# Performance work log

Measured on AMD Instinct MI355X. Metric: run time of the kernel, lower is better.

The kernel has to match this reference:

```python
import jax, jax.numpy as jnp
import numpy as np

D_MODEL = 512; D_INNER = 1024; D_STATE = 16; DT_RANK = 32; D_CONV = 4
N_LAYERS = 2; LSPP = 7; N_ROI = 2048; HIDDEN = 4096


def layer_norm(x, g, b, eps=1e-5):
    mu = x.mean(-1, keepdims=True)
    v = ((x - mu) ** 2).mean(-1, keepdims=True)
    return (x - mu) * jax.lax.rsqrt(v + eps) * g + b


def causal_dwconv(u, w, b):
    # u: [N,L,Di], w: [Di,K] depthwise, causal left-pad K-1
    x = jnp.transpose(u, (0, 2, 1))
    out = jax.lax.conv_general_dilated(x, w[:, None, :], (1,), [(D_CONV - 1, 0)],
                                       dimension_numbers=('NCH', 'OIH', 'NCH'),
                                       feature_group_count=D_INNER)
    return jnp.transpose(out, (0, 2, 1)) + b


def selective_scan(u, dt, A, B, C):
    # u, dt: [N,L,Di]; B, C: [N,L,S]; A: [Di,S]
    def step(h, xs):
        dt_t, B_t, C_t, u_t = xs
        dA = jnp.exp(dt_t[..., None] * A)                      # [N,Di,S]
        h = dA * h + (dt_t * u_t)[..., None] * B_t[:, None, :]
        return h, jnp.einsum('nds,ns->nd', h, C_t)
    h0 = jnp.zeros((u.shape[0], D_INNER, D_STATE), u.dtype)
    xs = (jnp.moveaxis(dt, 1, 0), jnp.moveaxis(B, 1, 0),
          jnp.moveaxis(C, 1, 0), jnp.moveaxis(u, 1, 0))
    _, ys = jax.lax.scan(step, h0, xs)
    return jnp.moveaxis(ys, 0, 1)                              # [N,L,Di]


def mamba_block(h, inw, cw, cb, xpw, dtw, dtb, Alog, Dp, ow):
    # decomposed bidirectional mamba ('dbm'): shared in_proj/gate, fwd+bwd scans summed
    xz = h @ inw.T                                             # [N,L,2*Di]
    xi, z = jnp.split(xz, 2, axis=-1)
    ys = []
    for d in range(2):
        u = xi if d == 0 else jnp.flip(xi, axis=1)
        u = jax.nn.silu(causal_dwconv(u, cw[d], cb[d]))
        dbl = u @ xpw[d].T                                     # [N,L,DT_RANK+2S]
        dtr = dbl[..., :DT_RANK]
        B = dbl[..., DT_RANK:DT_RANK + D_STATE]
        C = dbl[..., DT_RANK + D_STATE:]
        dt = jax.nn.softplus(dtr @ dtw[d].T + dtb[d])
        A = -jnp.exp(Alog[d])
        yd = selective_scan(u, dt, A, B, C) + u * Dp[d]
        ys.append(yd if d == 0 else jnp.flip(yd, axis=1))
    return ((ys[0] + ys[1]) * jax.nn.silu(z)) @ ow.T


def setup_inputs() -> dict:
    key = jax.random.key(0)
    ks = iter(jax.random.split(key, 40))
    rn = lambda shape, scale: jax.random.normal(next(ks), shape, dtype=jnp.float32) * scale
    inp = {}
    inp['x_flat'] = rn((N_ROI, D_MODEL * LSPP), 1.0)
    inp['conv_a_w'] = rn((256, 512, 3), (512 * 3) ** -0.5)
    inp['conv_p_w'] = rn((256, 512, 1), 512 ** -0.5)
    inp['se_w1'] = rn((32, 512), 512 ** -0.5)
    inp['se_b1'] = jnp.zeros((32,), jnp.float32)
    inp['se_w2'] = rn((512, 32), 32 ** -0.5)
    inp['se_b2'] = jnp.zeros((512,), jnp.float32)
    inp['ln_g'] = jnp.ones((N_LAYERS, D_MODEL), jnp.float32)
    inp['ln_b'] = jnp.zeros((N_LAYERS, D_MODEL), jnp.float32)
    inp['in_proj_w'] = rn((N_LAYERS, 2 * D_INNER, D_MODEL), D_MODEL ** -0.5)
    inp['conv_w'] = rn((N_LAYERS, 2, D_INNER, D_CONV), D_CONV ** -0.5)
    inp['conv_b'] = jnp.zeros((N_LAYERS, 2, D_INNER), jnp.float32)
    inp['x_proj_w'] = rn((N_LAYERS, 2, DT_RANK + 2 * D_STATE, D_INNER), D_INNER ** -0.5)
    inp['dt_proj_w'] = rn((N_LAYERS, 2, D_INNER, DT_RANK), DT_RANK ** -0.5)
    inp['dt_proj_b'] = rn((N_LAYERS, 2, D_INNER), 0.1) - 4.0
    inp['A_log'] = jnp.log(jnp.arange(1., D_STATE + 1., dtype=jnp.float32)) * jnp.ones((N_LAYERS, 2, D_INNER, D_STATE), jnp.float32)
    inp['D_param'] = jnp.ones((N_LAYERS, 2, D_INNER), jnp.float32)
    inp['out_proj_w'] = rn((N_LAYERS, D_MODEL, D_INNER), D_INNER ** -0.5)
    inp['out_ln_g'] = jnp.ones((D_MODEL,), jnp.float32)
    inp['out_ln_b'] = jnp.zeros((D_MODEL,), jnp.float32)
    inp['mlp_w1'] = rn((HIDDEN, D_MODEL), D_MODEL ** -0.5)
    inp['mlp_b1'] = jnp.zeros((HIDDEN,), jnp.float32)
    inp['mlp_w2'] = rn((HIDDEN, HIDDEN), HIDDEN ** -0.5)
    inp['mlp_b2'] = jnp.zeros((HIDDEN,), jnp.float32)
    return inp


def reference(x_flat, conv_a_w, conv_p_w, se_w1, se_b1, se_w2, se_b2, ln_g, ln_b,
              in_proj_w, conv_w, conv_b, x_proj_w, dt_proj_w, dt_proj_b, A_log,
              D_param, out_proj_w, out_ln_g, out_ln_b, mlp_w1, mlp_b1, mlp_w2, mlp_b2):
    N = x_flat.shape[0]
    x = x_flat.reshape(N, D_MODEL, LSPP)                       # [N,512,7]
    dn = ('NCH', 'OIH', 'NCH')
    # TSSE: strided conv branch + maxpool branch, concat, SE gating; L: 7 -> 4
    a = jax.nn.relu(jax.lax.conv_general_dilated(x, conv_a_w, (2,), [(1, 1)], dimension_numbers=dn))
    p = jax.lax.reduce_window(x, -jnp.inf, jax.lax.max, (1, 1, 3), (1, 1, 2), ((0, 0), (0, 0), (1, 1)))
    p = jax.nn.relu(jax.lax.conv_general_dilated(p, conv_p_w, (1,), [(0, 0)], dimension_numbers=dn))
    y = jnp.concatenate([a, p], axis=1)                        # [N,512,4]
    s = jax.nn.sigmoid(jax.nn.relu(y.mean(-1) @ se_w1.T + se_b1) @ se_w2.T + se_b2)
    y = y * s[:, :, None]
    # Mamba backbone: 2 pre-norm residual DBM blocks (mask is all-ones -> no-op)
    h = jnp.transpose(y, (0, 2, 1))                            # [N,L,512]
    for l in range(N_LAYERS):
        h = h + mamba_block(layer_norm(h, ln_g[l], ln_b[l]), in_proj_w[l], conv_w[l],
                            conv_b[l], x_proj_w[l], dt_proj_w[l], dt_proj_b[l],
                            A_log[l], D_param[l], out_proj_w[l])
    h = layer_norm(h, out_ln_g, out_ln_b)
    feat = h.mean(1)                                           # mean pool over time
    z1 = jax.nn.relu(feat @ mlp_w1.T + mlp_b1)
    return jax.nn.relu(z1 @ mlp_w2.T + mlp_b2)                 # [N,4096]
```

## Files before the change

### kernel.cpp

```cpp
#include <hip/hip_runtime.h>
#include <hip/hip_bf16.h>

typedef __hip_bfloat16 bf16;
typedef __attribute__((ext_vector_type(8))) short s16x8;
typedef __attribute__((ext_vector_type(4))) float f32x4;

__device__ __forceinline__ float u2f(unsigned short u){
  union { unsigned int i; float f; } v; v.i = ((unsigned int)u) << 16; return v.f;
}
__device__ __forceinline__ float bfu(bf16 x){ return __bfloat162float(x); }
__device__ __forceinline__ bf16  f2b(float x){ return __float2bfloat16(x); }

__device__ __forceinline__ void gload16(const void* g, void* l){
  __builtin_amdgcn_global_load_lds(
      (const __attribute__((address_space(1))) void*)g,
      (__attribute__((address_space(3))) void*)l, 16, 0, 0);
}

__device__ __forceinline__ float block_sum256(float v, float* red){
  #pragma unroll
  for (int o = 32; o > 0; o >>= 1) v += __shfl_down(v, o, 64);
  int lane = threadIdx.x & 63, wid = threadIdx.x >> 6;
  if (lane == 0) red[wid] = v;
  __syncthreads();
  float r = red[0] + red[1] + red[2] + red[3];
  __syncthreads();
  return r;
}

__global__ __launch_bounds__(256) void f2b4_kernel(
    const float4* __restrict__ in, ushort4* __restrict__ out, int n4)
{
  int stride = gridDim.x * 256;
  for (int i = blockIdx.x*256 + threadIdx.x; i < n4; i += stride){
    float4 v = in[i];
    ushort4 o;
    o.x = __bfloat16_as_ushort(f2b(v.x));
    o.y = __bfloat16_as_ushort(f2b(v.y));
    o.z = __bfloat16_as_ushort(f2b(v.z));
    o.w = __bfloat16_as_ushort(f2b(v.w));
    out[i] = o;
  }
}

__global__ __launch_bounds__(256) void xpw_pad_kernel(
    const float* __restrict__ xpw, bf16* __restrict__ out)
{
  int idx = blockIdx.x*256 + threadIdx.x;
  if (idx >= 524288) return;
  int l = idx >> 18, rem = idx & 262143, row = rem >> 10, c = rem & 1023;
  int d = row >> 7, r = row & 127;
  float v = (r < 64) ? xpw[(((size_t)l*2 + d)*64 + r)*1024 + c] : 0.f;
  out[idx] = f2b(v);
}

__global__ __launch_bounds__(256) void wdt_pad_kernel(
    const float* __restrict__ dtw, bf16* __restrict__ out)
{
  int idx = blockIdx.x*256 + threadIdx.x;
  if (idx >= 262144) return;
  int ld = idx >> 16, rem = idx & 65535, r = rem >> 6, c = rem & 63;
  float v = (c < 32) ? dtw[((size_t)ld*1024 + r)*32 + c] : 0.f;
  out[idx] = f2b(v);
}

__global__ __launch_bounds__(256) void atab_kernel(
    const float* __restrict__ Alog, float* __restrict__ Atab)
{
  int i = blockIdx.x*256 + threadIdx.x;
  if (i < 65536) Atab[i] = -__expf(Alog[i]) * 1.44269504088896f;
}

template<int ACT, int OMODE, bool HASBIAS>
__global__ __launch_bounds__(256) void mgemm_kernel(
    const bf16* __restrict__ A, const bf16* __restrict__ W,
    const float* __restrict__ bias, void* __restrict__ outp,
    int K, int ldo)
{
  __shared__ char lsA[16384];
  __shared__ char lsB[16384];
  const int tid = threadIdx.x;
  const int w = tid >> 6, l = tid & 63;
  const int nwg = gridDim.x * gridDim.y;
  const int lin = blockIdx.y * gridDim.x + blockIdx.x;
  const int cpx = nwg >> 3;
  const int swz = (lin & 7) * cpx + (lin >> 3);
  const int m0 = (swz % gridDim.x) * 128, n0 = (swz / gridDim.x) * 128;
  const int wr = w >> 1, wc = w & 1;
  const size_t ldb = (size_t)K * 2;
  const char* Ab = (const char*)A + (size_t)m0 * ldb;
  const char* Wb = (const char*)W + (size_t)n0 * ldb;

  const int srow = l >> 3;
  const int scb  = ((l & 7) ^ srow) << 4;
  const int fr = l & 15;
  const int fg = l >> 4;
  const int fsw = (fr & 7) << 4;

  f32x4 acc[4][4];
  #pragma unroll
  for (int m = 0; m < 4; ++m)
    #pragma unroll
    for (int n = 0; n < 4; ++n) acc[m][n] = (f32x4){0.f,0.f,0.f,0.f};

  const int nk = K >> 6;
  for (int kt = 0; kt < nk; ++kt){
    const char* As = Ab + (size_t)kt * 128;
    const char* Ws = Wb + (size_t)kt * 128;
    #pragma unroll
    for (int i = 0; i < 4; ++i){
      int row = (i*4 + w)*8 + srow;
      gload16(As + (size_t)row*ldb + scb, &lsA[(i*4 + w)*1024]);
    }
    #pragma unroll
    for (int i = 0; i < 4; ++i){
      int row = (i*4 + w)*8 + srow;
      gload16(Ws + (size_t)row*ldb + scb, &lsB[(i*4 + w)*1024]);
    }
    __syncthreads();

    s16x8 af[4][2], bfr[4][2];
    #pragma unroll
    for (int m = 0; m < 4; ++m){
      int row = wr*64 + m*16 + fr;
      af[m][0] = *(const s16x8*)&lsA[row*128 + (( 0 + fg*16) ^ fsw)];
      af[m][1] = *(const s16x8*)&lsA[row*128 + ((64 + fg*16) ^ fsw)];
    }
    #pragma unroll
    for (int n = 0; n < 4; ++n){
      int row = wc*64 + n*16 + fr;
      bfr[n][0] = *(const s16x8*)&lsB[row*128 + (( 0 + fg*16) ^ fsw)];
      bfr[n][1] = *(const s16x8*)&lsB[row*128 + ((64 + fg*16) ^ fsw)];
    }
    #pragma unroll
    for (int m = 0; m < 4; ++m)
      #pragma unroll
      for (int n = 0; n < 4; ++n){
        acc[m][n] = __builtin_amdgcn_mfma_f32_16x16x32_bf16(af[m][0], bfr[n][0], acc[m][n], 0, 0, 0);
        acc[m][n] = __builtin_amdgcn_mfma_f32_16x16x32_bf16(af[m][1], bfr[n][1], acc[m][n], 0, 0, 0);
      }
    __syncthreads();
  }

  const int orow0 = m0 + wr*64, ocol0 = n0 + wc*64;
  #pragma unroll
  for (int n = 0; n < 4; ++n){
    int col = ocol0 + n*16 + fr;
    float bv = HASBIAS ? bias[col] : 0.f;
    #pragma unroll
    for (int m = 0; m < 4; ++m){
      int rbase = orow0 + m*16 + fg*4;
      #pragma unroll
      for (int r = 0; r < 4; ++r){
        float v = acc[m][n][r] + bv;
        if (ACT == 1) v = fmaxf(v, 0.f);
        if (ACT == 2) v = (v > 20.f) ? v : log1pf(__expf(v));
        size_t oi = (size_t)(rbase + r) * ldo + col;
        if (OMODE == 0)      ((bf16*)outp)[oi] = f2b(v);
        else if (OMODE == 1) ((float*)outp)[oi] = v;
        else                 ((float*)outp)[oi] += v;
      }
    }
  }
}

__global__ __launch_bounds__(256) void bgemm_kernel(
    const bf16* __restrict__ A, const bf16* __restrict__ W,
    bf16* __restrict__ dtr_buf, float* __restrict__ dbl)
{
  __shared__ char lsA[16384];
  __shared__ char lsB[16384];
  const int tid = threadIdx.x;
  const int w = tid >> 6, l = tid & 63;
  const int nwg = gridDim.x * 2;
  const int lin = blockIdx.y * gridDim.x + blockIdx.x;
  const int cpx = nwg >> 3;
  const int swz = (lin & 7) * cpx + (lin >> 3);
  const int m0 = (swz % gridDim.x) * 128;
  const int d  = swz / gridDim.x;
  const int K = 1024;
  const int wr = w >> 1, wc = w & 1;
  const size_t ldb = (size_t)K * 2;
  const char* Ab = (const char*)(A + (size_t)d*8388608) + (size_t)m0 * ldb;
  const char* Wb = (const char*)(W + (size_t)d*131072);

  const int srow = l >> 3;
  const int scb  = ((l & 7) ^ srow) << 4;
  const int fr = l & 15;
  const int fg = l >> 4;
  const int fsw = (fr & 7) << 4;

  f32x4 acc[4][4];
  #pragma unroll
  for (int m = 0; m < 4; ++m)
    #pragma unroll
    for (int n = 0; n < 4; ++n) acc[m][n] = (f32x4){0.f,0.f,0.f,0.f};

  const int nk = K >> 6;
  for (int kt = 0; kt < nk; ++kt){
    const char* As = Ab + (size_t)kt * 128;
    const char* Ws = Wb + (size_t)kt * 128;
    #pragma unroll
    for (int i = 0; i < 4; ++i){
      int row = (i*4 + w)*8 + srow;
      gload16(As + (size_t)row*ldb + scb, &lsA[(i*4 + w)*1024]);
    }
    #pragma unroll
    for (int i = 0; i < 4; ++i){
      int row = (i*4 + w)*8 + srow;
      gload16(Ws + (size_t)row*ldb + scb, &lsB[(i*4 + w)*1024]);
    }
    __syncthreads();

    s16x8 af[4][2], bfr[4][2];
    #pragma unroll
    for (int m = 0; m < 4; ++m){
      int row = wr*64 + m*16 + fr;
      af[m][0] = *(const s16x8*)&lsA[row*128 + (( 0 + fg*16) ^ fsw)];
      af[m][1] = *(const s16x8*)&lsA[row*128 + ((64 + fg*16) ^ fsw)];
    }
    #pragma unroll
    for (int n = 0; n < 4; ++n){
      int row = wc*64 + n*16 + fr;
      bfr[n][0] = *(const s16x8*)&lsB[row*128 + (( 0 + fg*16) ^ fsw)];
      bfr[n][1] = *(const s16x8*)&lsB[row*128 + ((64 + fg*16) ^ fsw)];
    }
    #pragma unroll
    for (int m = 0; m < 4; ++m)
      #pragma unroll
      for (int n = 0; n < 4; ++n){
        acc[m][n] = __builtin_amdgcn_mfma_f32_16x16x32_bf16(af[m][0], bfr[n][0], acc[m][n], 0, 0, 0);
        acc[m][n] = __builtin_amdgcn_mfma_f32_16x16x32_bf16(af[m][1], bfr[n][1], acc[m][n], 0, 0, 0);
      }
    __syncthreads();
  }

  const int orow0 = m0 + wr*64, c0 = wc*64;
  #pragma unroll
  for (int n = 0; n < 4; ++n){
    int col = c0 + n*16 + fr;
    #pragma unroll
    for (int m = 0; m < 4; ++m){
      int rbase = orow0 + m*16 + fg*4;
      #pragma unroll
      for (int r = 0; r < 4; ++r){
        float v = acc[m][n][r];
        int row = rbase + r;
        if (col < 32)
          dtr_buf[((size_t)d*8192 + row)*64 + col] = f2b(v);
        else if (col < 64)
          dbl[(size_t)row*128 + d*64 + (col - 32)] = v;
        else if (col < 96)
          dtr_buf[((size_t)d*8192 + row)*64 + (col - 32)] = f2b(v);
      }
    }
  }
}

__global__ __launch_bounds__(256) void im2col_kernel(
    const float* __restrict__ x_flat, bf16* __restrict__ Aa, bf16* __restrict__ P)
{
  __shared__ float xs[512][8];
  const int n = blockIdx.x, tid = threadIdx.x;
  const float* xr = x_flat + (size_t)n * 3584;
  for (int i = tid; i < 3584; i += 256) xs[i / 7][i % 7] = xr[i];
  __syncthreads();
  bf16* Ar = Aa + (size_t)n * 4 * 1536;
  for (int i = tid; i < 6144; i += 256){
    int t = i / 1536, col = i - t*1536;
    int c = col / 3, kk = col - c*3;
    int p = 2*t - 1 + kk;
    float v = (p >= 0 && p < 7) ? xs[c][p] : 0.f;
    Ar[i] = f2b(v);
  }
  bf16* Pr = P + (size_t)n * 4 * 512;
  for (int i = tid; i < 2048; i += 256){
    int t = i >> 9, c = i & 511;
    int st = 2*t - 1;
    float m = -1e30f;
    #pragma unroll
    for (int k = 0; k < 3; ++k){ int p = st + k; if (p >= 0 && p < 7) m = fmaxf(m, xs[c][p]); }
    Pr[i] = f2b(m);
  }
}

__global__ __launch_bounds__(256) void se_kernel(
    const float* __restrict__ sw1, const float* __restrict__ sb1,
    const float* __restrict__ sw2, const float* __restrict__ sb2,
    float* __restrict__ h)
{
  __shared__ float yms[512];
  __shared__ float s1s[32];
  const int n = blockIdx.x, tid = threadIdx.x;
  float* hb = h + (size_t)n * 2048;
  for (int c = tid; c < 512; c += 256)
    yms[c] = 0.25f * (hb[c] + hb[512+c] + hb[1024+c] + hb[1536+c]);
  __syncthreads();
  {
    int o = tid >> 3, sl = tid & 7;
    const float* wr = sw1 + (size_t)o * 512 + sl*64;
    const float* ym = yms + sl*64;
    float a = 0.f;
    #pragma unroll 16
    for (int i = 0; i < 64; ++i) a += wr[i] * ym[i];
    a += __shfl_down(a, 4, 8);
    a += __shfl_down(a, 2, 8);
    a += __shfl_down(a, 1, 8);
    if (sl == 0) s1s[o] = fmaxf(a + sb1[o], 0.f);
  }
  __syncthreads();
  for (int c = tid; c < 512; c += 256){
    float a = sb2[c];
    const float* wr = sw2 + (size_t)c * 32;
    #pragma unroll
    for (int j = 0; j < 32; ++j) a += wr[j] * s1s[j];
    float s = 1.f / (1.f + __expf(-a));
    #pragma unroll
    for (int t = 0; t < 4; ++t) hb[t*512 + c] *= s;
  }
}

__global__ __launch_bounds__(256) void ln_kernel(
    const float* __restrict__ x, const float* __restrict__ g,
    const float* __restrict__ b, bf16* __restrict__ out)
{
  __shared__ float red[4];
  const int row = blockIdx.x, t = threadIdx.x;
  const float* xr = x + (size_t)row * 512;
  float v0 = xr[t], v1 = xr[t + 256];
  float s = block_sum256(v0 + v1, red);
  float mu = s * (1.f/512.f);
  float d0 = v0 - mu, d1 = v1 - mu;
  float sq = block_sum256(d0*d0 + d1*d1, red);
  float rstd = rsqrtf(sq * (1.f/512.f) + 1e-5f);
  out[(size_t)row*512 + t]       = f2b(d0*rstd*g[t]     + b[t]);
  out[(size_t)row*512 + t + 256] = f2b(d1*rstd*g[t+256] + b[t+256]);
}

__global__ __launch_bounds__(256) void finalln_kernel(
    const float* __restrict__ h, const float* __restrict__ g,
    const float* __restrict__ b, bf16* __restrict__ feat)
{
  __shared__ float red[4];
  const int n = blockIdx.x, t = threadIdx.x;
  float a0 = 0.f, a1 = 0.f;
  for (int tt = 0; tt < 4; ++tt){
    const float* xr = h + ((size_t)n*4 + tt)*512;
    float v0 = xr[t], v1 = xr[t+256];
    float s = block_sum256(v0 + v1, red);
    float mu = s * (1.f/512.f);
    float d0 = v0 - mu, d1 = v1 - mu;
    float sq = block_sum256(d0*d0 + d1*d1, red);
    float rstd = rsqrtf(sq * (1.f/512.f) + 1e-5f);
    a0 += d0*rstd*g[t]     + b[t];
    a1 += d1*rstd*g[t+256] + b[t+256];
  }
  feat[(size_t)n*512 + t]       = f2b(a0 * 0.25f);
  feat[(size_t)n*512 + t + 256] = f2b(a1 * 0.25f);
}

__global__ __launch_bounds__(256) void dwconv2_kernel(
    const bf16* __restrict__ xz, const float* __restrict__ cw,
    const float* __restrict__ cb, bf16* __restrict__ u)
{
  const int n = blockIdx.x;
  const int c4 = threadIdx.x * 4;
  ushort4 in4[4];
  #pragma unroll
  for (int t = 0; t < 4; ++t)
    in4[t] = *reinterpret_cast<const ushort4*>(&xz[((size_t)n*4 + t)*2048 + c4]);
  #pragma unroll
  for (int d = 0; d < 2; ++d){
    const float* cwd = cw + d*4096;
    const float* cbd = cb + d*1024;
    ushort4 out[4];
    #pragma unroll
    for (int j = 0; j < 4; ++j){
      float xa[4];
      #pragma unroll
      for (int t = 0; t < 4; ++t){
        int ts = d ? 3 - t : t;
        unsigned short us = j==0?in4[ts].x : j==1?in4[ts].y : j==2?in4[ts].z : in4[ts].w;
        xa[t] = u2f(us);
      }
      float4 wv = *reinterpret_cast<const float4*>(&cwd[(c4 + j)*4]);
      float bb = cbd[c4 + j];
      float o[4];
      o[0] = xa[0]*wv.w + bb;
      o[1] = xa[0]*wv.z + xa[1]*wv.w + bb;
      o[2] = xa[0]*wv.y + xa[1]*wv.z + xa[2]*wv.w + bb;
      o[3] = xa[0]*wv.x + xa[1]*wv.y + xa[2]*wv.z + xa[3]*wv.w + bb;
      #pragma unroll
      for (int t = 0; t < 4; ++t){
        float v = o[t];
        float sv = v / (1.f + __expf(-v));
        unsigned short us = __bfloat16_as_ushort(f2b(sv));
        if (j==0) out[t].x = us; else if (j==1) out[t].y = us;
        else if (j==2) out[t].z = us; else out[t].w = us;
      }
    }
    #pragma unroll
    for (int t = 0; t < 4; ++t)
      *reinterpret_cast<ushort4*>(&u[(size_t)d*8388608 + ((size_t)n*4 + t)*1024 + c4]) = out[t];
  }
}

__global__ __launch_bounds__(256) void scan2_kernel(
    const float* __restrict__ dbl, const bf16* __restrict__ dt2,
    const bf16* __restrict__ u, const bf16* __restrict__ xz,
    const float* __restrict__ Atab2, const float* __restrict__ Dp,
    bf16* __restrict__ gated)
{
  __shared__ float Bs[2][4][16], Cs[2][4][16];
  const int n = blockIdx.x, g = blockIdx.y, tid = threadIdx.x;
  {
    int t = tid >> 6, j = tid & 63;
    int d = j >> 5, jj = j & 31;
    float v = dbl[((size_t)n*4 + t)*128 + d*64 + jj];
    if (jj < 16) Bs[d][t][jj] = v; else Cs[d][t][jj-16] = v;
  }
  __syncthreads();
  const int c = g*256 + tid;
  const size_t base = (size_t)n*4*1024 + c;
  float yo0[4], yo1[4];
  float hs[16];
  {
    float A[16];
    const float4* ap = reinterpret_cast<const float4*>(Atab2 + (size_t)c*16);
    #pragma unroll
    for (int q = 0; q < 4; ++q){
      float4 v = ap[q];
      A[q*4+0]=v.x; A[q*4+1]=v.y; A[q*4+2]=v.z; A[q*4+3]=v.w;
    }
    const float Dpc = Dp[c];
    #pragma unroll
    for (int s = 0; s < 16; ++s) hs[s] = 0.f;
    #pragma unroll
    for (int t = 0; t < 4; ++t){
      float dtv = bfu(dt2[base + (size_t)t*1024]);
      float uv  = bfu(u  [base + (size_t)t*1024]);
      float du = dtv * uv;
      float yv = 0.f;
      #pragma unroll
      for (int s = 0; s < 16; ++s){
        float dA = __builtin_amdgcn_exp2f(dtv * A[s]);
        hs[s] = dA * hs[s] + du * Bs[0][t][s];
        yv += hs[s] * Cs[0][t][s];
      }
      yo0[t] = yv + uv * Dpc;
    }
  }
  {
    float A[16];
    const float4* ap = reinterpret_cast<const float4*>(Atab2 + 16384 + (size_t)c*16);
    #pragma unroll
    for (int q = 0; q < 4; ++q){
      float4 v = ap[q];
      A[q*4+0]=v.x; A[q*4+1]=v.y; A[q*4+2]=v.z; A[q*4+3]=v.w;
    }
    const float Dpc = Dp[1024 + c];
    #pragma unroll
    for (int s = 0; s < 16; ++s) hs[s] = 0.f;
    #pragma unroll
    for (int t = 0; t < 4; ++t){
      float dtv = bfu(dt2[8388608 + base + (size_t)t*1024]);
      float uv  = bfu(u  [8388608 + base + (size_t)t*1024]);
      float du = dtv * uv;
      float yv = 0.f;
      #pragma unroll
      for (int s = 0; s < 16; ++s){
        float dA = __builtin_amdgcn_exp2f(dtv * A[s]);
        hs[s] = dA * hs[s] + du * Bs[1][t][s];
        yv += hs[s] * Cs[1][t][s];
      }
      yo1[3 - t] = yv + uv * Dpc;
    }
  }
  #pragma unroll
  for (int t = 0; t < 4; ++t){
    float z = bfu(xz[(size_t)(n*4 + t)*2048 + 1024 + c]);
    float sv = z / (1.f + __expf(-z));
    gated[base + (size_t)t*1024] = f2b((yo0[t] + yo1[t]) * sv);
  }
}

extern "C" void kernel_launch(void* const* d_in, const int* in_sizes, int n_in,
                              void* d_out, int out_size, void* d_ws, size_t ws_size,
                              hipStream_t stream)
{
  const float* x_flat    = (const float*)d_in[0];
  const float* conv_a_w  = (const float*)d_in[1];
  const float* conv_p_w  = (const float*)d_in[2];
  const float* se_w1     = (const float*)d_in[3];
  const float* se_b1     = (const float*)d_in[4];
  const float* se_w2     = (const float*)d_in[5];
  const float* se_b2     = (const float*)d_in[6];
  const float* ln_g      = (const float*)d_in[7];
  const float* ln_b      = (const float*)d_in[8];
  const float* in_proj_w = (const float*)d_in[9];
  const float* conv_w    = (const float*)d_in[10];
  const float* conv_b    = (const float*)d_in[11];
  const float* x_proj_w  = (const float*)d_in[12];
  const float* dt_proj_w = (const float*)d_in[13];
  const float* dt_proj_b = (const float*)d_in[14];
  const float* A_log     = (const float*)d_in[15];
  const float* D_param   = (const float*)d_in[16];
  const float* out_proj_w= (const float*)d_in[17];
  const float* out_ln_g  = (const float*)d_in[18];
  const float* out_ln_b  = (const float*)d_in[19];
  const float* mlp_w1    = (const float*)d_in[20];
  const float* mlp_b1    = (const float*)d_in[21];
  const float* mlp_w2    = (const float*)d_in[22];
  const float* mlp_b2    = (const float*)d_in[23];

  char* ws = (char*)d_ws;
  const size_t OFF_H    = 0;
  const size_t OFF_HN   = OFF_H    + 16777216;
  const size_t OFF_XZ   = OFF_HN   + 8388608;
  const size_t OFF_U    = OFF_XZ   + 33554432;
  const size_t OFF_SCR  = OFF_U    + 33554432;
  const size_t OFF_YB   = OFF_SCR  + 25165824;
  const size_t OFF_WB   = OFF_YB   + 33554432;
  const size_t OFF_WXP  = OFF_WB   + 6291456;
  const size_t OFF_WDT  = OFF_WXP  + 1048576;
  const size_t OFF_ATAB = OFF_WDT  + 524288;

  float* h    = (float*)(ws + OFF_H);
  bf16*  hn   = (bf16*) (ws + OFF_HN);
  bf16*  xz   = (bf16*) (ws + OFF_XZ);
  bf16*  u    = (bf16*) (ws + OFF_U);
  float* dbl  = (float*)(ws + OFF_SCR);
  bf16*  dtrb = (bf16*) (ws + OFF_SCR + 4194304);
  bf16*  dt2  = (bf16*) (ws + OFF_YB);
  bf16*  feat = (bf16*) (ws + OFF_HN);
  bf16*  z1   = (bf16*) (ws + OFF_XZ);
  bf16*  wbi  = (bf16*) (ws + OFF_WB);
  bf16*  wbo  = (bf16*) (ws + OFF_WB + 4194304);
  bf16*  wxp  = (bf16*) (ws + OFF_WXP);
  bf16*  wdtp = (bf16*) (ws + OFF_WDT);
  float* Atab = (float*)(ws + OFF_ATAB);
  bf16*  wb1  = (bf16*) (ws + OFF_SCR);
  bf16*  wb2  = (bf16*) (ws + OFF_YB);
  bf16*  Aa   = (bf16*) (ws + OFF_SCR);
  bf16*  Pm   = (bf16*) (ws + OFF_YB);
  bf16*  wa   = (bf16*) (ws + OFF_YB + 8388608);
  bf16*  wp   = (bf16*) (ws + OFF_YB + 8388608 + 786432);
  float* outf = (float*)d_out;

  f2b4_kernel<<<512,  256, 0, stream>>>((const float4*)conv_a_w,   (ushort4*)wa,  98304);
  f2b4_kernel<<<256,  256, 0, stream>>>((const float4*)conv_p_w,   (ushort4*)wp,  32768);
  f2b4_kernel<<<2048, 256, 0, stream>>>((const float4*)in_proj_w,  (ushort4*)wbi, 524288);
  f2b4_kernel<<<1024, 256, 0, stream>>>((const float4*)out_proj_w, (ushort4*)wbo, 262144);
  xpw_pad_kernel<<<2048, 256, 0, stream>>>(x_proj_w, wxp);
  wdt_pad_kernel<<<1024, 256, 0, stream>>>(dt_proj_w, wdtp);
  atab_kernel<<<256, 256, 0, stream>>>(A_log, Atab);

  im2col_kernel<<<2048, 256, 0, stream>>>(x_flat, Aa, Pm);
  mgemm_kernel<1,1,false><<<dim3(64,2), 256, 0, stream>>>(
      Aa, wa, nullptr, h, 1536, 512);
  mgemm_kernel<1,1,false><<<dim3(64,2), 256, 0, stream>>>(
      Pm, wp, nullptr, (float*)h + 256, 512, 512);
  se_kernel<<<2048, 256, 0, stream>>>(se_w1, se_b1, se_w2, se_b2, h);

  for (int l = 0; l < 2; ++l){
    ln_kernel<<<8192, 256, 0, stream>>>(h, ln_g + l*512, ln_b + l*512, hn);
    mgemm_kernel<0,0,false><<<dim3(64,16), 256, 0, stream>>>(
        hn, wbi + (size_t)l*2048*512, nullptr, xz, 512, 2048);
    dwconv2_kernel<<<2048, 256, 0, stream>>>(
        xz, conv_w + (size_t)l*8192, conv_b + (size_t)l*2048, u);
    bgemm_kernel<<<dim3(64,2), 256, 0, stream>>>(
        u, wxp + (size_t)l*262144, dtrb, dbl);
    for (int d = 0; d < 2; ++d){
      int ld = l*2 + d;
      mgemm_kernel<2,0,true><<<dim3(64,8), 256, 0, stream>>>(
          dtrb + (size_t)d*8192*64, wdtp + (size_t)ld*65536,
          dt_proj_b + (size_t)ld*1024, dt2 + (size_t)d*8388608, 64, 1024);
    }
    scan2_kernel<<<dim3(2048,4), 256, 0, stream>>>(
        dbl, dt2, u, xz, Atab + (size_t)l*32768, D_param + (size_t)l*2048,
        u );
    mgemm_kernel<0,2,false><<<dim3(64,4), 256, 0, stream>>>(
        u, wbo + (size_t)l*512*1024, nullptr, h, 1024, 512);
  }

  finalln_kernel<<<2048, 256, 0, stream>>>(h, out_ln_g, out_ln_b, feat);

  f2b4_kernel<<<1024, 256, 0, stream>>>((const float4*)mlp_w1, (ushort4*)wb1, 524288);
  f2b4_kernel<<<2048, 256, 0, stream>>>((const float4*)mlp_w2, (ushort4*)wb2, 4194304);

  mgemm_kernel<1,0,true><<<dim3(16,32), 256, 0, stream>>>(
      feat, wb1, mlp_b1, z1, 512, 4096);
  mgemm_kernel<1,1,true><<<dim3(16,32), 256, 0, stream>>>(
      z1, wb2, mlp_b2, outf, 4096, 4096);
}
```

Measured before the change: 717.1 us.

## Fuse depthwise conv into x_proj GEMM and scan, batch prep and dt GEMMs

Removes the standalone depthwise-conv kernel and its intermediate u buffer. The conv plus SiLU is now computed inside the x_proj GEMM, which builds its A tile in LDS from xz instead of loading it, and recomputed again inside the scan kernel. The two per-direction dt_proj GEMMs are merged into one single-K-tile launch, and the many weight-conversion launches are merged into two prep kernels. This cuts launch count and global memory traffic for u, at the cost of redundant conv arithmetic and a synchronous, non-async A-tile fill in the x_proj GEMM.

```diff
diff --git a/kernel.cpp b/kernel.cpp
--- a/kernel.cpp
+++ b/kernel.cpp
@@ -28,47 +28,60 @@
   return r;
 }
 
-__global__ __launch_bounds__(256) void f2b4_kernel(
-    const float4* __restrict__ in, ushort4* __restrict__ out, int n4)
-{
-  int stride = gridDim.x * 256;
-  for (int i = blockIdx.x*256 + threadIdx.x; i < n4; i += stride){
-    float4 v = in[i];
-    ushort4 o;
-    o.x = __bfloat16_as_ushort(f2b(v.x));
-    o.y = __bfloat16_as_ushort(f2b(v.y));
-    o.z = __bfloat16_as_ushort(f2b(v.z));
-    o.w = __bfloat16_as_ushort(f2b(v.w));
-    out[i] = o;
-  }
-}
-
-__global__ __launch_bounds__(256) void xpw_pad_kernel(
-    const float* __restrict__ xpw, bf16* __restrict__ out)
-{
-  int idx = blockIdx.x*256 + threadIdx.x;
-  if (idx >= 524288) return;
-  int l = idx >> 18, rem = idx & 262143, row = rem >> 10, c = rem & 1023;
-  int d = row >> 7, r = row & 127;
-  float v = (r < 64) ? xpw[(((size_t)l*2 + d)*64 + r)*1024 + c] : 0.f;
-  out[idx] = f2b(v);
-}
-
-__global__ __launch_bounds__(256) void wdt_pad_kernel(
-    const float* __restrict__ dtw, bf16* __restrict__ out)
-{
-  int idx = blockIdx.x*256 + threadIdx.x;
-  if (idx >= 262144) return;
-  int ld = idx >> 16, rem = idx & 65535, r = rem >> 6, c = rem & 63;
-  float v = (c < 32) ? dtw[((size_t)ld*1024 + r)*32 + c] : 0.f;
-  out[idx] = f2b(v);
-}
-
-__global__ __launch_bounds__(256) void atab_kernel(
-    const float* __restrict__ Alog, float* __restrict__ Atab)
-{
-  int i = blockIdx.x*256 + threadIdx.x;
-  if (i < 65536) Atab[i] = -__expf(Alog[i]) * 1.44269504088896f;
+__device__ __forceinline__ ushort4 cvt4(float4 v){
+  ushort4 o;
+  o.x = __bfloat16_as_ushort(f2b(v.x));
+  o.y = __bfloat16_as_ushort(f2b(v.y));
+  o.z = __bfloat16_as_ushort(f2b(v.z));
+  o.w = __bfloat16_as_ushort(f2b(v.w));
+  return o;
+}
+
+__global__ __launch_bounds__(256) void prep_kernel(
+    const float* __restrict__ caw, const float* __restrict__ cpw,
+    const float* __restrict__ ipw, const float* __restrict__ opw,
+    const float* __restrict__ xpw, const float* __restrict__ dtw,
+    const float* __restrict__ alog,
+    bf16* __restrict__ wa, bf16* __restrict__ wp,
+    bf16* __restrict__ wbi, bf16* __restrict__ wbo,
+    bf16* __restrict__ wxp, bf16* __restrict__ wdtp,
+    float* __restrict__ atab)
+{
+  for (int i = blockIdx.x*256 + threadIdx.x; i < 1769472; i += gridDim.x*256){
+    if (i < 917504){
+      int j = i;
+      const float4* src; ushort4* dst;
+      if (j < 98304)      { src = (const float4*)caw; dst = (ushort4*)wa; }
+      else if (j < 131072){ j -= 98304;  src = (const float4*)cpw; dst = (ushort4*)wp; }
+      else if (j < 655360){ j -= 131072; src = (const float4*)ipw; dst = (ushort4*)wbi; }
+      else                { j -= 655360; src = (const float4*)opw; dst = (ushort4*)wbo; }
+      dst[j] = cvt4(src[j]);
+    } else if (i < 1441792){
+      int idx = i - 917504;
+      int l = idx >> 18, rem = idx & 262143, row = rem >> 10, c = rem & 1023;
+      int d = row >> 7, r = row & 127;
+      float v = (r < 64) ? xpw[(((size_t)l*2 + d)*64 + r)*1024 + c] : 0.f;
+      wxp[idx] = f2b(v);
+    } else if (i < 1703936){
+      int idx = i - 1441792;
+      int ld = idx >> 16, rem = idx & 65535, r = rem >> 6, cc = rem & 63;
+      float v = (cc < 32) ? dtw[((size_t)ld*1024 + r)*32 + cc] : 0.f;
+      wdtp[idx] = f2b(v);
+    } else {
+      int idx = i - 1703936;
+      atab[idx] = -__expf(alog[idx]) * 1.44269504088896f;
+    }
+  }
+}
+
+__global__ __launch_bounds__(256) void mlpprep_kernel(
+    const float4* __restrict__ w1, const float4* __restrict__ w2,
+    ushort4* __restrict__ o1, ushort4* __restrict__ o2)
+{
+  for (int i = blockIdx.x*256 + threadIdx.x; i < 4718592; i += gridDim.x*256){
+    if (i < 524288) o1[i] = cvt4(w1[i]);
+    else            o2[i - 524288] = cvt4(w2[i - 524288]);
+  }
 }
 
 template<int ACT, int OMODE, bool HASBIAS>
@@ -164,8 +177,9 @@
   }
 }
 
-__global__ __launch_bounds__(256) void bgemm_kernel(
-    const bf16* __restrict__ A, const bf16* __restrict__ W,
+__global__ __launch_bounds__(256) void bgemm2_kernel(
+    const bf16* __restrict__ xz, const bf16* __restrict__ W,
+    const float* __restrict__ cw, const float* __restrict__ cb,
     bf16* __restrict__ dtr_buf, float* __restrict__ dbl)
 {
   __shared__ char lsA[16384];
@@ -181,8 +195,10 @@
   const int K = 1024;
   const int wr = w >> 1, wc = w & 1;
   const size_t ldb = (size_t)K * 2;
-  const char* Ab = (const char*)(A + (size_t)d*8388608) + (size_t)m0 * ldb;
   const char* Wb = (const char*)(W + (size_t)d*131072);
+  const float* cwd = cw + d*4096;
+  const float* cbd = cb + d*1024;
+  const int n_base = m0 >> 2;
 
   const int srow = l >> 3;
   const int scb  = ((l & 7) ^ srow) << 4;
@@ -190,21 +206,50 @@
   const int fg = l >> 4;
   const int fsw = (fr & 7) << 4;
 
+  const int a_n  = tid >> 3;
+  const int a_j8 = tid & 7;
+
   f32x4 acc[4][4];
   #pragma unroll
   for (int m = 0; m < 4; ++m)
     #pragma unroll
     for (int n = 0; n < 4; ++n) acc[m][n] = (f32x4){0.f,0.f,0.f,0.f};
 
-  const int nk = K >> 6;
-  for (int kt = 0; kt < nk; ++kt){
-    const char* As = Ab + (size_t)kt * 128;
+  for (int kt = 0; kt < 16; ++kt){
+    const int ch = kt*64 + a_j8*8;
+    s16x8 xr[4];
+    #pragma unroll
+    for (int tp = 0; tp < 4; ++tp)
+      xr[tp] = *(const s16x8*)&xz[((size_t)(n_base + a_n)*4 + tp)*2048 + ch];
+    s16x8 ot[4];
+    #pragma unroll
+    for (int jj = 0; jj < 8; ++jj){
+      float xv[4];
+      #pragma unroll
+      for (int tp = 0; tp < 4; ++tp) xv[tp] = u2f((unsigned short)xr[tp][jj]);
+      float xa[4];
+      #pragma unroll
+      for (int tp = 0; tp < 4; ++tp) xa[tp] = d ? xv[3-tp] : xv[tp];
+      float4 w4 = *(const float4*)&cwd[(ch + jj)*4];
+      float bb = cbd[ch + jj];
+      float o[4];
+      o[0] = xa[0]*w4.w + bb;
+      o[1] = xa[0]*w4.z + xa[1]*w4.w + bb;
+      o[2] = xa[0]*w4.y + xa[1]*w4.z + xa[2]*w4.w + bb;
+      o[3] = xa[0]*w4.x + xa[1]*w4.y + xa[2]*w4.z + xa[3]*w4.w + bb;
+      #pragma unroll
+      for (int t = 0; t < 4; ++t){
+        float v = o[t];
+        float sv = v / (1.f + __expf(-v));
+        ot[t][jj] = (short)__bfloat16_as_ushort(f2b(sv));
+      }
+    }
+    #pragma unroll
+    for (int t = 0; t < 4; ++t){
+      int row = a_n*4 + t;
+      *(s16x8*)&lsA[row*128 + ((a_j8 << 4) ^ ((row & 7) << 4))] = ot[t];
+    }
     const char* Ws = Wb + (size_t)kt * 128;
-    #pragma unroll
-    for (int i = 0; i < 4; ++i){
-      int row = (i*4 + w)*8 + srow;
-      gload16(As + (size_t)row*ldb + scb, &lsA[(i*4 + w)*1024]);
-    }
     #pragma unroll
     for (int i = 0; i < 4; ++i){
       int row = (i*4 + w)*8 + srow;
@@ -252,6 +297,89 @@
           dbl[(size_t)row*128 + d*64 + (col - 32)] = v;
         else if (col < 96)
           dtr_buf[((size_t)d*8192 + row)*64 + (col - 32)] = f2b(v);
+      }
+    }
+  }
+}
+
+__global__ __launch_bounds__(256) void dtgemm_kernel(
+    const bf16* __restrict__ A, const bf16* __restrict__ W2,
+    const float* __restrict__ bias2, bf16* __restrict__ out2)
+{
+  __shared__ char lsA[16384];
+  __shared__ char lsB[16384];
+  const int tid = threadIdx.x;
+  const int w = tid >> 6, l = tid & 63;
+  const int nwg = gridDim.x * gridDim.y;
+  const int lin = blockIdx.y * gridDim.x + blockIdx.x;
+  const int cpx = nwg >> 3;
+  const int swz = (lin & 7) * cpx + (lin >> 3);
+  const int m0 = (swz % gridDim.x) * 128, n0 = (swz / gridDim.x) * 128;
+  const int d  = (m0 >= 8192) ? 1 : 0;
+  const int wr = w >> 1, wc = w & 1;
+  const size_t ldb = 128;
+  const char* Ab = (const char*)A + (size_t)m0 * ldb;
+  const char* Wb = (const char*)(W2 + (size_t)d*65536) + (size_t)n0 * ldb;
+  const float* bias = bias2 + d*1024;
+  bf16* outp = out2 + (size_t)d*8388608;
+
+  const int srow = l >> 3;
+  const int scb  = ((l & 7) ^ srow) << 4;
+  const int fr = l & 15, fg = l >> 4;
+  const int fsw = (fr & 7) << 4;
+
+  f32x4 acc[4][4];
+  #pragma unroll
+  for (int m = 0; m < 4; ++m)
+    #pragma unroll
+    for (int n = 0; n < 4; ++n) acc[m][n] = (f32x4){0.f,0.f,0.f,0.f};
+
+  #pragma unroll
+  for (int i = 0; i < 4; ++i){
+    int row = (i*4 + w)*8 + srow;
+    gload16(Ab + (size_t)row*ldb + scb, &lsA[(i*4 + w)*1024]);
+  }
+  #pragma unroll
+  for (int i = 0; i < 4; ++i){
+    int row = (i*4 + w)*8 + srow;
+    gload16(Wb + (size_t)row*ldb + scb, &lsB[(i*4 + w)*1024]);
+  }
+  __syncthreads();
+
+  s16x8 af[4][2], bfr[4][2];
+  #pragma unroll
+  for (int m = 0; m < 4; ++m){
+    int row = wr*64 + m*16 + fr;
+    af[m][0] = *(const s16x8*)&lsA[row*128 + (( 0 + fg*16) ^ fsw)];
+    af[m][1] = *(const s16x8*)&lsA[row*128 + ((64 + fg*16) ^ fsw)];
+  }
+  #pragma unroll
+  for (int n = 0; n < 4; ++n){
+    int row = wc*64 + n*16 + fr;
+    bfr[n][0] = *(const s16x8*)&lsB[row*128 + (( 0 + fg*16) ^ fsw)];
+    bfr[n][1] = *(const s16x8*)&lsB[row*128 + ((64 + fg*16) ^ fsw)];
+  }
+  #pragma unroll
+  for (int m = 0; m < 4; ++m)
+    #pragma unroll
+    for (int n = 0; n < 4; ++n){
+      acc[m][n] = __builtin_amdgcn_mfma_f32_16x16x32_bf16(af[m][0], bfr[n][0], acc[m][n], 0, 0, 0);
+      acc[m][n] = __builtin_amdgcn_mfma_f32_16x16x32_bf16(af[m][1], bfr[n][1], acc[m][n], 0, 0, 0);
+    }
+
+  const int orow0 = (m0 - d*8192) + wr*64, ocol0 = n0 + wc*64;
+  #pragma unroll
+  for (int n = 0; n < 4; ++n){
+    int col = ocol0 + n*16 + fr;
+    float bv = bias[col];
+    #pragma unroll
+    for (int m = 0; m < 4; ++m){
+      int rbase = orow0 + m*16 + fg*4;
+      #pragma unroll
+      for (int r = 0; r < 4; ++r){
+        float v = acc[m][n][r] + bv;
+        v = (v > 20.f) ? v : log1pf(__expf(v));
+        outp[(size_t)(rbase + r) * 1024 + col] = f2b(v);
       }
     }
   }
@@ -359,57 +487,11 @@
   feat[(size_t)n*512 + t + 256] = f2b(a1 * 0.25f);
 }
 
-__global__ __launch_bounds__(256) void dwconv2_kernel(
-    const bf16* __restrict__ xz, const float* __restrict__ cw,
-    const float* __restrict__ cb, bf16* __restrict__ u)
-{
-  const int n = blockIdx.x;
-  const int c4 = threadIdx.x * 4;
-  ushort4 in4[4];
-  #pragma unroll
-  for (int t = 0; t < 4; ++t)
-    in4[t] = *reinterpret_cast<const ushort4*>(&xz[((size_t)n*4 + t)*2048 + c4]);
-  #pragma unroll
-  for (int d = 0; d < 2; ++d){
-    const float* cwd = cw + d*4096;
-    const float* cbd = cb + d*1024;
-    ushort4 out[4];
-    #pragma unroll
-    for (int j = 0; j < 4; ++j){
-      float xa[4];
-      #pragma unroll
-      for (int t = 0; t < 4; ++t){
-        int ts = d ? 3 - t : t;
-        unsigned short us = j==0?in4[ts].x : j==1?in4[ts].y : j==2?in4[ts].z : in4[ts].w;
-        xa[t] = u2f(us);
-      }
-      float4 wv = *reinterpret_cast<const float4*>(&cwd[(c4 + j)*4]);
-      float bb = cbd[c4 + j];
-      float o[4];
-      o[0] = xa[0]*wv.w + bb;
-      o[1] = xa[0]*wv.z + xa[1]*wv.w + bb;
-      o[2] = xa[0]*wv.y + xa[1]*wv.z + xa[2]*wv.w + bb;
-      o[3] = xa[0]*wv.x + xa[1]*wv.y + xa[2]*wv.z + xa[3]*wv.w + bb;
-      #pragma unroll
-      for (int t = 0; t < 4; ++t){
-        float v = o[t];
-        float sv = v / (1.f + __expf(-v));
-        unsigned short us = __bfloat16_as_ushort(f2b(sv));
-        if (j==0) out[t].x = us; else if (j==1) out[t].y = us;
-        else if (j==2) out[t].z = us; else out[t].w = us;
-      }
-    }
-    #pragma unroll
-    for (int t = 0; t < 4; ++t)
-      *reinterpret_cast<ushort4*>(&u[(size_t)d*8388608 + ((size_t)n*4 + t)*1024 + c4]) = out[t];
-  }
-}
-
 __global__ __launch_bounds__(256) void scan2_kernel(
     const float* __restrict__ dbl, const bf16* __restrict__ dt2,
-    const bf16* __restrict__ u, const bf16* __restrict__ xz,
-    const float* __restrict__ Atab2, const float* __restrict__ Dp,
-    bf16* __restrict__ gated)
+    const bf16* __restrict__ xz, const float* __restrict__ cw,
+    const float* __restrict__ cb, const float* __restrict__ Atab2,
+    const float* __restrict__ Dp, bf16* __restrict__ gated)
 {
   __shared__ float Bs[2][4][16], Cs[2][4][16];
   const int n = blockIdx.x, g = blockIdx.y, tid = threadIdx.x;
@@ -422,6 +504,26 @@
   __syncthreads();
   const int c = g*256 + tid;
   const size_t base = (size_t)n*4*1024 + c;
+  float xv[4];
+  #pragma unroll
+  for (int t = 0; t < 4; ++t) xv[t] = bfu(xz[((size_t)(n*4 + t))*2048 + c]);
+  float4 w0 = *(const float4*)&cw[(size_t)c*4];
+  float4 w1 = *(const float4*)&cw[4096 + (size_t)c*4];
+  float b0v = cb[c], b1v = cb[1024 + c];
+  float uu0[4], uu1[4];
+  uu0[0] = xv[0]*w0.w + b0v;
+  uu0[1] = xv[0]*w0.z + xv[1]*w0.w + b0v;
+  uu0[2] = xv[0]*w0.y + xv[1]*w0.z + xv[2]*w0.w + b0v;
+  uu0[3] = xv[0]*w0.x + xv[1]*w0.y + xv[2]*w0.z + xv[3]*w0.w + b0v;
+  uu1[0] = xv[3]*w1.w + b1v;
+  uu1[1] = xv[3]*w1.z + xv[2]*w1.w + b1v;
+  uu1[2] = xv[3]*w1.y + xv[2]*w1.z + xv[1]*w1.w + b1v;
+  uu1[3] = xv[3]*w1.x + xv[2]*w1.y + xv[1]*w1.z + xv[0]*w1.w + b1v;
+  #pragma unroll
+  for (int t = 0; t < 4; ++t){
+    uu0[t] = uu0[t] / (1.f + __expf(-uu0[t]));
+    uu1[t] = uu1[t] / (1.f + __expf(-uu1[t]));
+  }
   float yo0[4], yo1[4];
   float hs[16];
   {
@@ -438,8 +540,7 @@
     #pragma unroll
     for (int t = 0; t < 4; ++t){
       float dtv = bfu(dt2[base + (size_t)t*1024]);
-      float uv  = bfu(u  [base + (size_t)t*1024]);
-      float du = dtv * uv;
+      float du = dtv * uu0[t];
       float yv = 0.f;
       #pragma unroll
       for (int s = 0; s < 16; ++s){
@@ -447,7 +548,7 @@
         hs[s] = dA * hs[s] + du * Bs[0][t][s];
         yv += hs[s] * Cs[0][t][s];
       }
-      yo0[t] = yv + uv * Dpc;
+      yo0[t] = yv + uu0[t] * Dpc;
     }
   }
   {
@@ -464,8 +565,7 @@
     #pragma unroll
     for (int t = 0; t < 4; ++t){
       float dtv = bfu(dt2[8388608 + base + (size_t)t*1024]);
-      float uv  = bfu(u  [8388608 + base + (size_t)t*1024]);
-      float du = dtv * uv;
+      float du = dtv * uu1[t];
       float yv = 0.f;
       #pragma unroll
       for (int s = 0; s < 16; ++s){
@@ -473,7 +573,7 @@
         hs[s] = dA * hs[s] + du * Bs[1][t][s];
         yv += hs[s] * Cs[1][t][s];
       }
-      yo1[3 - t] = yv + uv * Dpc;
+      yo1[3 - t] = yv + uu1[t] * Dpc;
     }
   }
   #pragma unroll
@@ -528,7 +628,7 @@
   float* h    = (float*)(ws + OFF_H);
   bf16*  hn   = (bf16*) (ws + OFF_HN);
   bf16*  xz   = (bf16*) (ws + OFF_XZ);
-  bf16*  u    = (bf16*) (ws + OFF_U);
+  bf16*  gated= (bf16*) (ws + OFF_U);
   float* dbl  = (float*)(ws + OFF_SCR);
   bf16*  dtrb = (bf16*) (ws + OFF_SCR + 4194304);
   bf16*  dt2  = (bf16*) (ws + OFF_YB);
@@ -547,13 +647,9 @@
   bf16*  wp   = (bf16*) (ws + OFF_YB + 8388608 + 786432);
   float* outf = (float*)d_out;
 
-  f2b4_kernel<<<512,  256, 0, stream>>>((const float4*)conv_a_w,   (ushort4*)wa,  98304);
-  f2b4_kernel<<<256,  256, 0, stream>>>((const float4*)conv_p_w,   (ushort4*)wp,  32768);
-  f2b4_kernel<<<2048, 256, 0, stream>>>((const float4*)in_proj_w,  (ushort4*)wbi, 524288);
-  f2b4_kernel<<<1024, 256, 0, stream>>>((const float4*)out_proj_w, (ushort4*)wbo, 262144);
-  xpw_pad_kernel<<<2048, 256, 0, stream>>>(x_proj_w, wxp);
-  wdt_pad_kernel<<<1024, 256, 0, stream>>>(dt_proj_w, wdtp);
-  atab_kernel<<<256, 256, 0, stream>>>(A_log, Atab);
+  prep_kernel<<<2048, 256, 0, stream>>>(
+      conv_a_w, conv_p_w, in_proj_w, out_proj_w, x_proj_w, dt_proj_w, A_log,
+      wa, wp, wbi, wbo, wxp, wdtp, Atab);
 
   im2col_kernel<<<2048, 256, 0, stream>>>(x_flat, Aa, Pm);
   mgemm_kernel<1,1,false><<<dim3(64,2), 256, 0, stream>>>(
@@ -563,30 +659,26 @@
   se_kernel<<<2048, 256, 0, stream>>>(se_w1, se_b1, se_w2, se_b2, h);
 
   for (int l = 0; l < 2; ++l){
+    const float* cw_l = conv_w + (size_t)l*8192;
+    const float* cb_l = conv_b + (size_t)l*2048;
     ln_kernel<<<8192, 256, 0, stream>>>(h, ln_g + l*512, ln_b + l*512, hn);
     mgemm_kernel<0,0,false><<<dim3(64,16), 256, 0, stream>>>(
         hn, wbi + (size_t)l*2048*512, nullptr, xz, 512, 2048);
-    dwconv2_kernel<<<2048, 256, 0, stream>>>(
-        xz, conv_w + (size_t)l*8192, conv_b + (size_t)l*2048, u);
-    bgemm_kernel<<<dim3(64,2), 256, 0, stream>>>(
-        u, wxp + (size_t)l*262144, dtrb, dbl);
-    for (int d = 0; d < 2; ++d){
-      int ld = l*2 + d;
-      mgemm_kernel<2,0,true><<<dim3(64,8), 256, 0, stream>>>(
-          dtrb + (size_t)d*8192*64, wdtp + (size_t)ld*65536,
-          dt_proj_b + (size_t)ld*1024, dt2 + (size_t)d*8388608, 64, 1024);
-    }
+    bgemm2_kernel<<<dim3(64,2), 256, 0, stream>>>(
+        xz, wxp + (size_t)l*262144, cw_l, cb_l, dtrb, dbl);
+    dtgemm_kernel<<<dim3(128,8), 256, 0, stream>>>(
+        dtrb, wdtp + (size_t)l*131072, dt_proj_b + (size_t)l*2048, dt2);
     scan2_kernel<<<dim3(2048,4), 256, 0, stream>>>(
-        dbl, dt2, u, xz, Atab + (size_t)l*32768, D_param + (size_t)l*2048,
-        u );
+        dbl, dt2, xz, cw_l, cb_l, Atab + (size_t)l*32768,
+        D_param + (size_t)l*2048, gated);
     mgemm_kernel<0,2,false><<<dim3(64,4), 256, 0, stream>>>(
-        u, wbo + (size_t)l*512*1024, nullptr, h, 1024, 512);
+        gated, wbo + (size_t)l*512*1024, nullptr, h, 1024, 512);
   }
 
   finalln_kernel<<<2048, 256, 0, stream>>>(h, out_ln_g, out_ln_b, feat);
 
-  f2b4_kernel<<<1024, 256, 0, stream>>>((const float4*)mlp_w1, (ushort4*)wb1, 524288);
-  f2b4_kernel<<<2048, 256, 0, stream>>>((const float4*)mlp_w2, (ushort4*)wb2, 4194304);
+  mlpprep_kernel<<<4096, 256, 0, stream>>>(
+      (const float4*)mlp_w1, (const float4*)mlp_w2, (ushort4*)wb1, (ushort4*)wb2);
 
   mgemm_kernel<1,0,true><<<dim3(16,32), 256, 0, stream>>>(
       feat, wb1, mlp_b1, z1, 512, 4096);
```

Result: no change. 715.3 us (-0.3%).
